# Kernel optimization log

Hardware: AMD Instinct MI355X
Metric: run time of the kernel (lower is better)

## Reference

```python
import jax, jax.numpy as jnp
import numpy as np

N_NODES = 50000
N_EDGES = 800000
NFEAT, NHID, NCLASS, NCLUSTER = 512, 64, 16, 32


def gcn_conv(x, W, b, edge_index, edge_weight, n):
    """PyG GCNConv: add self-loops, symmetric normalization, linear + scatter-add."""
    row, col = edge_index[0], edge_index[1]
    loop = jnp.arange(n, dtype=row.dtype)
    row = jnp.concatenate([row, loop])
    col = jnp.concatenate([col, loop])
    w = jnp.concatenate([edge_weight, jnp.ones((n,), dtype=edge_weight.dtype)])
    # degree computed on target index (gcn_norm convention)
    deg = jax.ops.segment_sum(w, col, num_segments=n)
    dinv = jnp.where(deg > 0, jax.lax.rsqrt(deg), 0.0)
    norm = dinv[row] * w * dinv[col]          # [E+n]
    xw = x @ W                                # [n, out]
    msg = xw[row] * norm[:, None]             # gather + scale
    out = jax.ops.segment_sum(msg, col, num_segments=n)  # scatter-add
    return out + b


def setup_inputs() -> dict:
    key = jax.random.key(0)
    ks = jax.random.split(key, 12)
    def glorot(k, fan_in, fan_out):
        s = np.sqrt(6.0 / (fan_in + fan_out)).astype(np.float32)
        return jax.random.uniform(k, (fan_in, fan_out), jnp.float32, -s, s)
    x = jax.random.normal(ks[0], (N_NODES, NFEAT), jnp.float32)
    edge_index = jax.random.randint(ks[1], (2, N_EDGES), 0, N_NODES, dtype=jnp.int64)
    edge_weight = jax.random.uniform(ks[2], (N_EDGES,), jnp.float32)
    return {
        "x": x, "edge_index": edge_index, "edge_weight": edge_weight,
        "W1": glorot(ks[3], NFEAT, NHID), "b1": jnp.zeros((NHID,), jnp.float32),
        "W2": glorot(ks[4], NHID, NHID), "b2": jnp.zeros((NHID,), jnp.float32),
        "fcW1": glorot(ks[5], NHID, NCLASS), "fcb1": jnp.zeros((NCLASS,), jnp.float32),
        "fcW2": glorot(ks[6], NHID, NCLUSTER), "fcb2": jnp.zeros((NCLUSTER,), jnp.float32),
    }


def reference(x, edge_index, edge_weight, W1, b1, W2, b2, fcW1, fcb1, fcW2, fcb2):
    n = x.shape[0]
    h = jax.nn.relu(gcn_conv(x, W1, b1, edge_index, edge_weight, n))
    # dropout omitted (eval-mode / deterministic reference)
    h = gcn_conv(h, W2, b2, edge_index, edge_weight, n)
    pred = h @ fcW1 + fcb1
    pred_cluster = h @ fcW2 + fcb2
    return (pred, pred_cluster)
```

## Files before the change

kernel.cpp:

```cpp
#include <hip/hip_runtime.h>
#include <hip/hip_bf16.h>
#include <cstdint>
#include <cstddef>

#define N_FEAT 512
#define N_HID 64
#define N_CLASS 16
#define N_CLUSTER 32
#define NPART 8

typedef short short8 __attribute__((ext_vector_type(8)));
typedef float floatx4 __attribute__((ext_vector_type(4)));
typedef unsigned short u16;
typedef unsigned short u16x4 __attribute__((ext_vector_type(4)));

__device__ __forceinline__ short f2bf(float f) {
  __hip_bfloat16 h = __float2bfloat16(f);
  return *reinterpret_cast<short*>(&h);
}
__device__ __forceinline__ u16 f2bfu(float f) { return (u16)f2bf(f); }
__device__ __forceinline__ float bf2f(u16 u) {
  return __uint_as_float((unsigned)u << 16);
}

__device__ __forceinline__ void prepBF_one(const float* __restrict__ W,
                                           short* __restrict__ BF, int K, int idx) {
  int lane = idx & 63;
  int sj = idx >> 6;
  int j = sj & 3, s = sj >> 2;
  int col = j * 16 + (lane & 15);
  int k0 = s * 32 + ((lane >> 4) << 3);
  short8 v;
  #pragma unroll
  for (int t = 0; t < 8; ++t) v[t] = f2bf(W[(size_t)(k0 + t) * 64 + col]);
  *(short8*)(BF + (size_t)idx * 8) = v;
}

__global__ void k_init(uint4* __restrict__ h16, int n16,
                       const float* __restrict__ W1, short* __restrict__ BF1,
                       const float* __restrict__ W2, short* __restrict__ BF2,
                       int nbZ) {
  int b = blockIdx.x, t = threadIdx.x;
  if (b < nbZ) {
    int i = b * 256 + t;
    if (i < n16) h16[i] = make_uint4(0u, 0u, 0u, 0u);
  } else if (b < nbZ + 16) {
    prepBF_one(W1, BF1, N_FEAT, (b - nbZ) * 256 + t);
  } else {
    int idx = (b - nbZ - 16) * 256 + t;
    if (idx < 512) prepBF_one(W2, BF2, N_HID, idx);
  }
}

__global__ void k_degcnt2(const int* __restrict__ col, const float* __restrict__ w,
                          unsigned long long* __restrict__ hist, int H, int E) {
  int e = blockIdx.x * 256 + threadIdx.x;
  if (e >= E) return;
  int p = blockIdx.x & (NPART - 1);
  int c = col[e];
  unsigned long long fx = (unsigned long long)__float2uint_rn(w[e] * 16777216.0f);
  atomicAdd(&hist[(size_t)p * H + c], (1ull << 40) | fx);
}

__global__ __launch_bounds__(256) void k_redscan(
    const unsigned long long* __restrict__ hist, int H,
    float* __restrict__ dinv, int* __restrict__ off,
    int* __restrict__ bsum, int n) {
  __shared__ int sh[256];
  int t = threadIdx.x;
  int i = blockIdx.x * 256 + t;
  int v = 0;
  if (i < n) {
    unsigned long long tot = 0;
    #pragma unroll
    for (int p = 0; p < NPART; ++p) tot += hist[(size_t)p * H + i];
    v = (int)(tot >> 40);
    float wsum = (float)(tot & ((1ull << 40) - 1)) * 5.9604644775390625e-08f;
    dinv[i] = rsqrtf(1.0f + wsum);
  }
  sh[t] = v;
  __syncthreads();
  #pragma unroll
  for (int d = 1; d < 256; d <<= 1) {
    int x = 0;
    if (t >= d) x = sh[t - d];
    __syncthreads();
    if (t >= d) sh[t] += x;
    __syncthreads();
  }
  if (i < n) off[i] = sh[t] - v;
  if (t == 255) bsum[blockIdx.x] = sh[255];
}

__global__ __launch_bounds__(256) void k_scan2(const int* __restrict__ bsum,
                                               int* __restrict__ bsum2, int nb) {
  __shared__ int sh[256];
  int t = threadIdx.x;
  int v = (t < nb) ? bsum[t] : 0;
  sh[t] = v;
  __syncthreads();
  #pragma unroll
  for (int d = 1; d < 256; d <<= 1) {
    int x = 0;
    if (t >= d) x = sh[t - d];
    __syncthreads();
    if (t >= d) sh[t] += x;
    __syncthreads();
  }
  if (t < nb) bsum2[t] = sh[t] - v;
}

__global__ void k_scan3_initcur(int* __restrict__ off, const int* __restrict__ bsum2,
                                const unsigned long long* __restrict__ hist, int H,
                                int* __restrict__ cur, int n, int E) {
  int i = blockIdx.x * 256 + threadIdx.x;
  if (i < n) {
    int o = off[i] + bsum2[blockIdx.x];
    off[i] = o;
    int running = o;
    #pragma unroll
    for (int p = 0; p < NPART; ++p) {
      cur[(size_t)p * H + i] = running;
      running += (int)(hist[(size_t)p * H + i] >> 40);
    }
  }
  if (i == 0) off[n] = E;
}

__device__ __forceinline__ void gemm_wave(
    const float* __restrict__ A, const short8* __restrict__ BF,
    u16* __restrict__ C, int M, int tile) {
  const int lane = threadIdx.x & 63;
  const int rbase = tile * 16;
  int r = rbase + (lane & 15);
  if (r >= M) r = M - 1;
  const float* arow = A + (size_t)r * 512 + ((lane >> 4) << 3);
  const short8* bbase = BF + lane;

  float4 pa0[4], pa1[4];
  short8 pb[2][4];
  #pragma unroll
  for (int s = 0; s < 4; ++s) {
    pa0[s] = *(const float4*)(arow + s * 32);
    pa1[s] = *(const float4*)(arow + s * 32 + 4);
  }
  #pragma unroll
  for (int s = 0; s < 2; ++s)
    #pragma unroll
    for (int j = 0; j < 4; ++j)
      pb[s][j] = bbase[(s * 4 + j) * 64];
  __builtin_amdgcn_sched_barrier(0);

  floatx4 acc[4];
  #pragma unroll
  for (int j = 0; j < 4; ++j) acc[j] = (floatx4){0.f, 0.f, 0.f, 0.f};

  #pragma unroll
  for (int s = 0; s < 16; ++s) {
    const int sa = s & 3;
    const int sb = s & 1;
    float4 a0 = pa0[sa], a1 = pa1[sa];
    short8 af;
    af[0] = f2bf(a0.x); af[1] = f2bf(a0.y); af[2] = f2bf(a0.z); af[3] = f2bf(a0.w);
    af[4] = f2bf(a1.x); af[5] = f2bf(a1.y); af[6] = f2bf(a1.z); af[7] = f2bf(a1.w);
    acc[0] = __builtin_amdgcn_mfma_f32_16x16x32_bf16(af, pb[sb][0], acc[0], 0, 0, 0);
    acc[1] = __builtin_amdgcn_mfma_f32_16x16x32_bf16(af, pb[sb][1], acc[1], 0, 0, 0);
    acc[2] = __builtin_amdgcn_mfma_f32_16x16x32_bf16(af, pb[sb][2], acc[2], 0, 0, 0);
    acc[3] = __builtin_amdgcn_mfma_f32_16x16x32_bf16(af, pb[sb][3], acc[3], 0, 0, 0);
    if (s + 4 < 16) {
      pa0[sa] = *(const float4*)(arow + (s + 4) * 32);
      pa1[sa] = *(const float4*)(arow + (s + 4) * 32 + 4);
    }
    if (s + 2 < 16) {
      #pragma unroll
      for (int j = 0; j < 4; ++j)
        pb[sb][j] = bbase[((s + 2) * 4 + j) * 64];
    }
    __builtin_amdgcn_sched_barrier(0);
  }

  const int srow = rbase + (lane >> 4) * 4;
  const int scol = lane & 15;
  #pragma unroll
  for (int i = 0; i < 4; ++i) {
    int rr = srow + i;
    if (rr < M) {
      #pragma unroll
      for (int j = 0; j < 4; ++j)
        C[(size_t)rr * 64 + j * 16 + scol] = f2bfu(acc[j][i]);
    }
  }
}

__device__ __forceinline__ void fill_block(
    int f, const int* __restrict__ rowi, const int* __restrict__ coli,
    const float* __restrict__ w, const float* __restrict__ dinv,
    int* __restrict__ cur, int H, unsigned* __restrict__ pairs, int E) {
  int e = f * 256 + threadIdx.x;
  if (e >= E) return;
  int p = f & (NPART - 1);
  int r = rowi[e], c = coli[e];
  int pos = atomicAdd(&cur[(size_t)p * H + c], 1);
  pairs[pos] = ((unsigned)r << 16) | (u16)f2bf(dinv[r] * w[e] * dinv[c]);
}

__global__ __launch_bounds__(256, 4) void k_gemmfill(
    const float* __restrict__ A, const short8* __restrict__ BF,
    u16* __restrict__ C, int M, int nbT,
    const int* __restrict__ rowi, const int* __restrict__ coli,
    const float* __restrict__ w, const float* __restrict__ dinv,
    int* __restrict__ cur, int H, unsigned* __restrict__ pairs, int E) {
  const int q = blockIdx.x / 5;
  const int r = blockIdx.x % 5;
  if (r == 0) {
    int tile = q * 4 + (threadIdx.x >> 6);
    if (tile < nbT) gemm_wave(A, BF, C, M, tile);
  } else {
    fill_block(q * 4 + (r - 1), rowi, coli, w, dinv, cur, H, pairs, E);
  }
}

__global__ __launch_bounds__(64, 4) void k_mfma64(
    const u16* __restrict__ Av, const short8* __restrict__ BF,
    u16* __restrict__ C, int M) {
  const int lane = threadIdx.x & 63;
  const int rbase = blockIdx.x * 16;
  int r = rbase + (lane & 15);
  if (r >= M) r = M - 1;
  const int klo = (lane >> 4) * 8;
  const u16* arow = Av + (size_t)r * 64 + klo;
  const short8* bbase = BF + lane;

  short8 pah[2];
  short8 pb[2][4];
  pah[0] = *(const short8*)(arow);
  pah[1] = *(const short8*)(arow + 32);
  #pragma unroll
  for (int s = 0; s < 2; ++s)
    #pragma unroll
    for (int j = 0; j < 4; ++j)
      pb[s][j] = bbase[(s * 4 + j) * 64];

  floatx4 acc[4];
  #pragma unroll
  for (int j = 0; j < 4; ++j) acc[j] = (floatx4){0.f, 0.f, 0.f, 0.f};

  #pragma unroll
  for (int s = 0; s < 2; ++s) {
    acc[0] = __builtin_amdgcn_mfma_f32_16x16x32_bf16(pah[s], pb[s][0], acc[0], 0, 0, 0);
    acc[1] = __builtin_amdgcn_mfma_f32_16x16x32_bf16(pah[s], pb[s][1], acc[1], 0, 0, 0);
    acc[2] = __builtin_amdgcn_mfma_f32_16x16x32_bf16(pah[s], pb[s][2], acc[2], 0, 0, 0);
    acc[3] = __builtin_amdgcn_mfma_f32_16x16x32_bf16(pah[s], pb[s][3], acc[3], 0, 0, 0);
  }

  const int srow = rbase + (lane >> 4) * 4;
  const int scol = lane & 15;
  #pragma unroll
  for (int i = 0; i < 4; ++i) {
    int rr = srow + i;
    if (rr < M) {
      #pragma unroll
      for (int j = 0; j < 4; ++j)
        C[(size_t)rr * 64 + j * 16 + scol] = f2bfu(acc[j][i]);
    }
  }
}

template<bool RELU>
__global__ __launch_bounds__(256) void k_gather(
    const int* __restrict__ off, const unsigned* __restrict__ pairs,
    const float* __restrict__ dinv,
    const u16* __restrict__ xw, const float* __restrict__ bias,
    u16* __restrict__ h, int n) {
  int gid = blockIdx.x * 256 + threadIdx.x;
  int c = gid >> 6, lane = gid & 63;
  if (c >= n) return;
  float s = dinv[c]; s *= s;
  float acc = fmaf(bf2f(xw[(size_t)c * 64 + lane]), s, bias[lane]);
  int i = off[c], end = off[c + 1];
  for (; i + 7 < end; i += 8) {
    unsigned p[8];
    float v[8];
    #pragma unroll
    for (int t = 0; t < 8; ++t) p[t] = pairs[i + t];
    #pragma unroll
    for (int t = 0; t < 8; ++t)
      v[t] = bf2f(xw[(size_t)(p[t] >> 16) * 64 + lane]);
    #pragma unroll
    for (int t = 0; t < 8; ++t)
      acc = fmaf(v[t], __uint_as_float((p[t] & 0xffffu) << 16), acc);
  }
  for (; i + 1 < end; i += 2) {
    unsigned p0 = pairs[i], p1 = pairs[i + 1];
    float v0 = bf2f(xw[(size_t)(p0 >> 16) * 64 + lane]);
    float v1 = bf2f(xw[(size_t)(p1 >> 16) * 64 + lane]);
    acc = fmaf(v0, __uint_as_float((p0 & 0xffffu) << 16), acc);
    acc = fmaf(v1, __uint_as_float((p1 & 0xffffu) << 16), acc);
  }
  if (i < end) {
    unsigned p = pairs[i];
    acc = fmaf(bf2f(xw[(size_t)(p >> 16) * 64 + lane]),
               __uint_as_float((p & 0xffffu) << 16), acc);
  }
  if (RELU) acc = fmaxf(acc, 0.f);
  h[(size_t)c * 64 + lane] = f2bfu(acc);
}

__global__ __launch_bounds__(256) void k_fc(
    const u16* __restrict__ h,
    const float* __restrict__ fW1, const float* __restrict__ fb1,
    const float* __restrict__ fW2, const float* __restrict__ fb2,
    float* __restrict__ out, int M) {
  __shared__ float Hs[64][68];
  __shared__ float Ws[64][48];
  __shared__ float bs[48];
  const int t = threadIdx.x;
  const int row0 = blockIdx.x * 64;
  #pragma unroll
  for (int i = 0; i < 4; ++i) {
    int f = t + i * 256;
    int r = f >> 4, k4 = f & 15;
    int rr = row0 + r;
    float4 v = make_float4(0.f, 0.f, 0.f, 0.f);
    if (rr < M) {
      u16x4 u = *(const u16x4*)&h[(size_t)rr * 64 + k4 * 4];
      v = make_float4(bf2f(u[0]), bf2f(u[1]), bf2f(u[2]), bf2f(u[3]));
    }
    *(float4*)&Hs[r][k4 * 4] = v;
  }
  for (int f = t; f < 64 * 48; f += 256) {
    int k = f / 48, c = f - k * 48;
    Ws[k][c] = (c < 16) ? fW1[k * 16 + c] : fW2[k * 32 + (c - 16)];
  }
  if (t < 48) bs[t] = (t < 16) ? fb1[t] : fb2[t - 16];
  __syncthreads();
  const int tr = t >> 4, tc = t & 15;
  float acc[4][3] = {{0.f}};
  #pragma unroll 8
  for (int k = 0; k < 64; ++k) {
    float a[4], b[3];
    #pragma unroll
    for (int i = 0; i < 4; ++i) a[i] = Hs[tr * 4 + i][k];
    #pragma unroll
    for (int j = 0; j < 3; ++j) b[j] = Ws[k][tc * 3 + j];
    #pragma unroll
    for (int i = 0; i < 4; ++i)
      #pragma unroll
      for (int j = 0; j < 3; ++j) acc[i][j] = fmaf(a[i], b[j], acc[i][j]);
  }
  #pragma unroll
  for (int i = 0; i < 4; ++i) {
    int rr = row0 + tr * 4 + i;
    if (rr >= M) continue;
    #pragma unroll
    for (int j = 0; j < 3; ++j) {
      int c = tc * 3 + j;
      float v = acc[i][j] + bs[c];
      if (c < 16) out[(size_t)rr * 16 + c] = v;
      else out[(size_t)M * 16 + (size_t)rr * 32 + (c - 16)] = v;
    }
  }
}

extern "C" void kernel_launch(void* const* d_in, const int* in_sizes, int n_in,
                              void* d_out, int out_size, void* d_ws, size_t ws_size,
                              hipStream_t stream) {
  const float* x    = (const float*)d_in[0];
  const int*   ei   = (const int*)d_in[1];
  const float* ew   = (const float*)d_in[2];
  const float* W1   = (const float*)d_in[3];
  const float* b1   = (const float*)d_in[4];
  const float* W2   = (const float*)d_in[5];
  const float* b2   = (const float*)d_in[6];
  const float* fW1  = (const float*)d_in[7];
  const float* fb1  = (const float*)d_in[8];
  const float* fW2  = (const float*)d_in[9];
  const float* fb2  = (const float*)d_in[10];
  float* out = (float*)d_out;

  const int N = in_sizes[0] / N_FEAT;
  const int E = in_sizes[2];
  const int H = (N + 63) & ~63;
  const int* row = ei;
  const int* col = ei + E;

  char* ws = (char*)d_ws;
  float*              dinv = (float*)(ws + 0x000000);
  int*                off  = (int*)  (ws + 0x080000);
  int*                bsum = (int*)  (ws + 0x0C0000);
  int*                bsum2= (int*)  (ws + 0x0C1000);
  short*              BF1  = (short*)(ws + 0x0C8000);
  short*              BF2  = (short*)(ws + 0x0DA000);
  unsigned long long* hist = (unsigned long long*)(ws + 0x100000);
  int*                cur  = (int*)  (ws + 0x500000);
  unsigned*           pairs= (unsigned*)(ws + 0x6C0000);
  u16*                bufA = (u16*)  (ws + 0xD40000);
  u16*                bufB = (u16*)  (ws + 0x1980000);

  const int nbN  = (N + 255) / 256;
  const int nbE  = (E + 255) / 256;
  const int nbT  = (N + 15) / 16;
  const int nGB  = (nbT + 3) / 4;
  const int nbG  = (N + 63) / 64;
  const int nbW  = (N * 64 + 255) / 256;
  const int nH16 = NPART * H / 2;
  const int nbZ  = (nH16 + 255) / 256;

  k_init<<<nbZ + 18, 256, 0, stream>>>((uint4*)hist, nH16, W1, BF1, W2, BF2, nbZ);

  k_degcnt2<<<nbE, 256, 0, stream>>>(col, ew, hist, H, E);
  k_redscan<<<nbN, 256, 0, stream>>>(hist, H, dinv, off, bsum, N);
  k_scan2  <<<1,   256, 0, stream>>>(bsum, bsum2, nbN);
  k_scan3_initcur<<<nbN, 256, 0, stream>>>(off, bsum2, hist, H, cur, N, E);

  k_gemmfill<<<5 * nGB, 256, 0, stream>>>(
      x, (const short8*)BF1, bufA, N, nbT,
      row, col, ew, dinv, cur, H, pairs, E);

  k_gather<true><<<nbW, 256, 0, stream>>>(off, pairs, dinv, bufA, b1, bufB, N);

  k_mfma64<<<nbT, 64, 0, stream>>>(bufB, (const short8*)BF2, bufA, N);
  k_gather<false><<<nbW, 256, 0, stream>>>(off, pairs, dinv, bufA, b2, bufB, N);

  k_fc<<<nbG, 256, 0, stream>>>(bufB, fW1, fb1, fW2, fb2, out, N);
}
```

Measured before the change: 188.8 us.

## Split fused gemm/fill kernel and stage X tile through swizzled LDS

```diff
diff --git a/kernel.cpp b/kernel.cpp
--- a/kernel.cpp
+++ b/kernel.cpp
@@ -127,96 +127,86 @@
   if (i == 0) off[n] = E;
 }
 
-__device__ __forceinline__ void gemm_wave(
+__global__ void k_fill2(const int* __restrict__ rowi, const int* __restrict__ coli,
+                        const float* __restrict__ w, const float* __restrict__ dinv,
+                        int* __restrict__ cur, int H,
+                        unsigned* __restrict__ pairs, int E) {
+  int e = blockIdx.x * 256 + threadIdx.x;
+  if (e >= E) return;
+  int p = blockIdx.x & (NPART - 1);
+  int r = rowi[e], c = coli[e];
+  int pos = atomicAdd(&cur[(size_t)p * H + c], 1);
+  pairs[pos] = ((unsigned)r << 16) | (u16)f2bf(dinv[r] * w[e] * dinv[c]);
+}
+
+__global__ __launch_bounds__(512, 4) void k_gemm512L(
     const float* __restrict__ A, const short8* __restrict__ BF,
-    u16* __restrict__ C, int M, int tile) {
-  const int lane = threadIdx.x & 63;
-  const int rbase = tile * 16;
-  int r = rbase + (lane & 15);
-  if (r >= M) r = M - 1;
-  const float* arow = A + (size_t)r * 512 + ((lane >> 4) << 3);
+    u16* __restrict__ C, int M) {
+  __shared__ u16 Ls[64 * 512];
+  const int t = threadIdx.x;
+  const int row0 = blockIdx.x * 64;
+
+  float4 va[16];
+  #pragma unroll
+  for (int j = 0; j < 16; ++j) {
+    int rl = j * 4 + (t >> 7);
+    int grow = row0 + rl;
+    if (grow >= M) grow = M - 1;
+    va[j] = *(const float4*)(A + (size_t)grow * 512 + (t & 127) * 4);
+  }
+  __builtin_amdgcn_sched_barrier(0);
+  #pragma unroll
+  for (int j = 0; j < 16; ++j) {
+    int rl = j * 4 + (t >> 7);
+    int k16 = (t & 127) >> 1;
+    int pk = k16 ^ (rl & 7);
+    u16x4 o;
+    o[0] = f2bfu(va[j].x); o[1] = f2bfu(va[j].y);
+    o[2] = f2bfu(va[j].z); o[3] = f2bfu(va[j].w);
+    *(u16x4*)(Ls + rl * 512 + pk * 8 + (t & 1) * 4) = o;
+  }
+  __syncthreads();
+
+  const int lane = t & 63;
+  const int w = t >> 6;
+  const int t4 = w & 3, ch = w >> 2;
+  const int row_r = t4 * 16 + (lane & 15);
+  const int xr = row_r & 7;
   const short8* bbase = BF + lane;
 
-  float4 pa0[4], pa1[4];
-  short8 pb[2][4];
-  #pragma unroll
-  for (int s = 0; s < 4; ++s) {
-    pa0[s] = *(const float4*)(arow + s * 32);
-    pa1[s] = *(const float4*)(arow + s * 32 + 4);
-  }
-  #pragma unroll
-  for (int s = 0; s < 2; ++s)
-    #pragma unroll
-    for (int j = 0; j < 4; ++j)
-      pb[s][j] = bbase[(s * 4 + j) * 64];
-  __builtin_amdgcn_sched_barrier(0);
-
-  floatx4 acc[4];
-  #pragma unroll
-  for (int j = 0; j < 4; ++j) acc[j] = (floatx4){0.f, 0.f, 0.f, 0.f};
+  short8 pb[2][2];
+  #pragma unroll
+  for (int s = 0; s < 2; ++s) {
+    pb[s][0] = bbase[(s * 4 + 2 * ch) * 64];
+    pb[s][1] = bbase[(s * 4 + 2 * ch + 1) * 64];
+  }
+
+  floatx4 acc[2];
+  acc[0] = (floatx4){0.f, 0.f, 0.f, 0.f};
+  acc[1] = (floatx4){0.f, 0.f, 0.f, 0.f};
 
   #pragma unroll
   for (int s = 0; s < 16; ++s) {
-    const int sa = s & 3;
     const int sb = s & 1;
-    float4 a0 = pa0[sa], a1 = pa1[sa];
-    short8 af;
-    af[0] = f2bf(a0.x); af[1] = f2bf(a0.y); af[2] = f2bf(a0.z); af[3] = f2bf(a0.w);
-    af[4] = f2bf(a1.x); af[5] = f2bf(a1.y); af[6] = f2bf(a1.z); af[7] = f2bf(a1.w);
+    int k16 = s * 4 + (lane >> 4);
+    short8 af = *(const short8*)(Ls + row_r * 512 + (k16 ^ xr) * 8);
     acc[0] = __builtin_amdgcn_mfma_f32_16x16x32_bf16(af, pb[sb][0], acc[0], 0, 0, 0);
     acc[1] = __builtin_amdgcn_mfma_f32_16x16x32_bf16(af, pb[sb][1], acc[1], 0, 0, 0);
-    acc[2] = __builtin_amdgcn_mfma_f32_16x16x32_bf16(af, pb[sb][2], acc[2], 0, 0, 0);
-    acc[3] = __builtin_amdgcn_mfma_f32_16x16x32_bf16(af, pb[sb][3], acc[3], 0, 0, 0);
-    if (s + 4 < 16) {
-      pa0[sa] = *(const float4*)(arow + (s + 4) * 32);
-      pa1[sa] = *(const float4*)(arow + (s + 4) * 32 + 4);
-    }
     if (s + 2 < 16) {
-      #pragma unroll
-      for (int j = 0; j < 4; ++j)
-        pb[sb][j] = bbase[((s + 2) * 4 + j) * 64];
-    }
-    __builtin_amdgcn_sched_barrier(0);
-  }
-
-  const int srow = rbase + (lane >> 4) * 4;
-  const int scol = lane & 15;
+      pb[sb][0] = bbase[((s + 2) * 4 + 2 * ch) * 64];
+      pb[sb][1] = bbase[((s + 2) * 4 + 2 * ch + 1) * 64];
+    }
+  }
+
+  const int srow = row0 + t4 * 16 + (lane >> 4) * 4;
+  const int scol = 2 * ch * 16 + (lane & 15);
   #pragma unroll
   for (int i = 0; i < 4; ++i) {
     int rr = srow + i;
     if (rr < M) {
-      #pragma unroll
-      for (int j = 0; j < 4; ++j)
-        C[(size_t)rr * 64 + j * 16 + scol] = f2bfu(acc[j][i]);
-    }
-  }
-}
-
-__device__ __forceinline__ void fill_block(
-    int f, const int* __restrict__ rowi, const int* __restrict__ coli,
-    const float* __restrict__ w, const float* __restrict__ dinv,
-    int* __restrict__ cur, int H, unsigned* __restrict__ pairs, int E) {
-  int e = f * 256 + threadIdx.x;
-  if (e >= E) return;
-  int p = f & (NPART - 1);
-  int r = rowi[e], c = coli[e];
-  int pos = atomicAdd(&cur[(size_t)p * H + c], 1);
-  pairs[pos] = ((unsigned)r << 16) | (u16)f2bf(dinv[r] * w[e] * dinv[c]);
-}
-
-__global__ __launch_bounds__(256, 4) void k_gemmfill(
-    const float* __restrict__ A, const short8* __restrict__ BF,
-    u16* __restrict__ C, int M, int nbT,
-    const int* __restrict__ rowi, const int* __restrict__ coli,
-    const float* __restrict__ w, const float* __restrict__ dinv,
-    int* __restrict__ cur, int H, unsigned* __restrict__ pairs, int E) {
-  const int q = blockIdx.x / 5;
-  const int r = blockIdx.x % 5;
-  if (r == 0) {
-    int tile = q * 4 + (threadIdx.x >> 6);
-    if (tile < nbT) gemm_wave(A, BF, C, M, tile);
-  } else {
-    fill_block(q * 4 + (r - 1), rowi, coli, w, dinv, cur, H, pairs, E);
+      C[(size_t)rr * 64 + scol]      = f2bfu(acc[0][i]);
+      C[(size_t)rr * 64 + scol + 16] = f2bfu(acc[1][i]);
+    }
   }
 }
 
@@ -399,8 +389,8 @@
 
   const int nbN  = (N + 255) / 256;
   const int nbE  = (E + 255) / 256;
+  const int nbS  = (N + 63) / 64;
   const int nbT  = (N + 15) / 16;
-  const int nGB  = (nbT + 3) / 4;
   const int nbG  = (N + 63) / 64;
   const int nbW  = (N * 64 + 255) / 256;
   const int nH16 = NPART * H / 2;
@@ -412,11 +402,9 @@
   k_redscan<<<nbN, 256, 0, stream>>>(hist, H, dinv, off, bsum, N);
   k_scan2  <<<1,   256, 0, stream>>>(bsum, bsum2, nbN);
   k_scan3_initcur<<<nbN, 256, 0, stream>>>(off, bsum2, hist, H, cur, N, E);
-
-  k_gemmfill<<<5 * nGB, 256, 0, stream>>>(
-      x, (const short8*)BF1, bufA, N, nbT,
-      row, col, ew, dinv, cur, H, pairs, E);
-
+  k_fill2  <<<nbE, 256, 0, stream>>>(row, col, ew, dinv, cur, H, pairs, E);
+
+  k_gemm512L<<<nbS, 512, 0, stream>>>(x, (const short8*)BF1, bufA, N);
   k_gather<true><<<nbW, 256, 0, stream>>>(off, pairs, dinv, bufA, b1, bufB, N);
 
   k_mfma64<<<nbT, 64, 0, stream>>>(bufB, (const short8*)BF2, bufA, N);
```

Result: slower. 193.7 us (+2.6%).

## Split first GEMM across degree-count and fill passes, record edge ranks

Applied to the files above, without the earlier changes.

```diff
diff --git a/kernel.cpp b/kernel.cpp
--- a/kernel.cpp
+++ b/kernel.cpp
@@ -50,16 +50,6 @@
     int idx = (b - nbZ - 16) * 256 + t;
     if (idx < 512) prepBF_one(W2, BF2, N_HID, idx);
   }
-}
-
-__global__ void k_degcnt2(const int* __restrict__ col, const float* __restrict__ w,
-                          unsigned long long* __restrict__ hist, int H, int E) {
-  int e = blockIdx.x * 256 + threadIdx.x;
-  if (e >= E) return;
-  int p = blockIdx.x & (NPART - 1);
-  int c = col[e];
-  unsigned long long fx = (unsigned long long)__float2uint_rn(w[e] * 16777216.0f);
-  atomicAdd(&hist[(size_t)p * H + c], (1ull << 40) | fx);
 }
 
 __global__ __launch_bounds__(256) void k_redscan(
@@ -192,31 +182,35 @@
   }
 }
 
-__device__ __forceinline__ void fill_block(
-    int f, const int* __restrict__ rowi, const int* __restrict__ coli,
-    const float* __restrict__ w, const float* __restrict__ dinv,
-    int* __restrict__ cur, int H, unsigned* __restrict__ pairs, int E) {
-  int e = f * 256 + threadIdx.x;
-  if (e >= E) return;
-  int p = f & (NPART - 1);
-  int r = rowi[e], c = coli[e];
-  int pos = atomicAdd(&cur[(size_t)p * H + c], 1);
-  pairs[pos] = ((unsigned)r << 16) | (u16)f2bf(dinv[r] * w[e] * dinv[c]);
-}
-
-__global__ __launch_bounds__(256, 4) void k_gemmfill(
+template<int MODE>
+__global__ __launch_bounds__(256, 4) void k_fused(
     const float* __restrict__ A, const short8* __restrict__ BF,
-    u16* __restrict__ C, int M, int nbT,
+    u16* __restrict__ C, int M, int nbT, int tile0, int S,
     const int* __restrict__ rowi, const int* __restrict__ coli,
-    const float* __restrict__ w, const float* __restrict__ dinv,
-    int* __restrict__ cur, int H, unsigned* __restrict__ pairs, int E) {
-  const int q = blockIdx.x / 5;
-  const int r = blockIdx.x % 5;
+    const float* __restrict__ w,
+    unsigned long long* __restrict__ hist, int* __restrict__ rank,
+    const float* __restrict__ dinv, const int* __restrict__ cur,
+    unsigned* __restrict__ pairs, int H, int E) {
+  const int q = blockIdx.x / (S + 1);
+  const int r = blockIdx.x % (S + 1);
   if (r == 0) {
-    int tile = q * 4 + (threadIdx.x >> 6);
+    int tile = tile0 + q * 4 + (threadIdx.x >> 6);
     if (tile < nbT) gemm_wave(A, BF, C, M, tile);
   } else {
-    fill_block(q * 4 + (r - 1), rowi, coli, w, dinv, cur, H, pairs, E);
+    int f = q * S + (r - 1);
+    int e = f * 256 + threadIdx.x;
+    if (e >= E) return;
+    int p = f & (NPART - 1);
+    int c = coli[e];
+    if constexpr (MODE == 0) {
+      unsigned long long fx = (unsigned long long)__float2uint_rn(w[e] * 16777216.0f);
+      unsigned long long old = atomicAdd(&hist[(size_t)p * H + c], (1ull << 40) | fx);
+      rank[e] = (int)(old >> 40);
+    } else {
+      int rr = rowi[e];
+      int pos = cur[(size_t)p * H + c] + rank[e];
+      pairs[pos] = ((unsigned)rr << 16) | (u16)f2bf(dinv[rr] * w[e] * dinv[c]);
+    }
   }
 }
 
@@ -394,28 +388,37 @@
   unsigned long long* hist = (unsigned long long*)(ws + 0x100000);
   int*                cur  = (int*)  (ws + 0x500000);
   unsigned*           pairs= (unsigned*)(ws + 0x6C0000);
+  int*                rank = (int*)  (ws + 0xA00000);
   u16*                bufA = (u16*)  (ws + 0xD40000);
   u16*                bufB = (u16*)  (ws + 0x1980000);
 
   const int nbN  = (N + 255) / 256;
   const int nbE  = (E + 255) / 256;
   const int nbT  = (N + 15) / 16;
-  const int nGB  = (nbT + 3) / 4;
   const int nbG  = (N + 63) / 64;
   const int nbW  = (N * 64 + 255) / 256;
   const int nH16 = NPART * H / 2;
   const int nbZ  = (nH16 + 255) / 256;
 
+  const int GA = 160;
+  const int SA = (nbE + GA - 1) / GA;
+  const int tilesA = GA * 4;
+  const int GB = (nbT - tilesA + 3) / 4;
+  const int SB = (nbE + GB - 1) / GB;
+
   k_init<<<nbZ + 18, 256, 0, stream>>>((uint4*)hist, nH16, W1, BF1, W2, BF2, nbZ);
 
-  k_degcnt2<<<nbE, 256, 0, stream>>>(col, ew, hist, H, E);
+  k_fused<0><<<GA * (SA + 1), 256, 0, stream>>>(
+      x, (const short8*)BF1, bufA, N, nbT, 0, SA,
+      row, col, ew, hist, rank, dinv, cur, pairs, H, E);
+
   k_redscan<<<nbN, 256, 0, stream>>>(hist, H, dinv, off, bsum, N);
   k_scan2  <<<1,   256, 0, stream>>>(bsum, bsum2, nbN);
   k_scan3_initcur<<<nbN, 256, 0, stream>>>(off, bsum2, hist, H, cur, N, E);
 
-  k_gemmfill<<<5 * nGB, 256, 0, stream>>>(
-      x, (const short8*)BF1, bufA, N, nbT,
-      row, col, ew, dinv, cur, H, pairs, E);
+  k_fused<1><<<GB * (SB + 1), 256, 0, stream>>>(
+      x, (const short8*)BF1, bufA, N, nbT, tilesA, SB,
+      row, col, ew, hist, rank, dinv, cur, pairs, H, E);
 
   k_gather<true><<<nbW, 256, 0, stream>>>(off, pairs, dinv, bufA, b1, bufB, N);
 
```

Result: no change. 186.0 us (-1.5%).
